# Optimization experiments

Hardware: AMD Instinct MI355X
Metric: run time of the kernel (lower is better)

The kernel has to match this reference:

```python
import jax, jax.numpy as jnp
import numpy as np

B, N, V, H = 8, 2048, 256, 1024
EPS = 1e-5
NEG = -1e9


def _layernorm(x, g, b):
    m = jnp.mean(x, axis=-1, keepdims=True)
    v = jnp.mean((x - m) ** 2, axis=-1, keepdims=True)
    return (x - m) / jnp.sqrt(v + EPS) * g + b


def setup_inputs() -> dict:
    key = jax.random.key(0)
    ks = jax.random.split(key, 10)
    tril = jnp.tril(jnp.ones((N, N), jnp.float32))
    return {
        "h": jax.random.normal(ks[0], (B, N, V), jnp.float32),
        "mask_one": tril,                      # keep causal entries
        "mask_zero": NEG * (1.0 - tril),       # -inf-ish above diagonal
        "ln_attn_g": jnp.ones((V,), jnp.float32),
        "ln_attn_b": jnp.zeros((V,), jnp.float32),
        "ln_mlp_g": jnp.ones((V,), jnp.float32),
        "ln_mlp_b": jnp.zeros((V,), jnp.float32),
        "wv": jax.random.normal(ks[1], (V,), jnp.float32),
        "wv_bos": jax.random.normal(ks[2], (V,), jnp.float32),
        "wo_w": jax.random.normal(ks[3], (V, V), jnp.float32) / np.sqrt(V),
        "qk_bos": jax.random.normal(ks[4], (V,), jnp.float32),
        "qk_previous": jax.random.normal(ks[5], (V,), jnp.float32),
        "qk_direction": jnp.ones((V,), jnp.float32),  # middel_layer=False, frozen
        "w1": jax.random.normal(ks[6], (H, V), jnp.float32) / np.sqrt(V),
        "w2": jax.random.normal(ks[7], (V, H), jnp.float32) / np.sqrt(H),
    }


def reference(h, mask_one, mask_zero, ln_attn_g, ln_attn_b, ln_mlp_g, ln_mlp_b,
              wv, wv_bos, wo_w, qk_bos, qk_previous, qk_direction, w1, w2):
    b, n, v = h.shape
    # mask blends LayerNorm only into row 0 (BOS position)
    attn_input = h.at[:, 0, :].set(_layernorm(h[:, 0, :], ln_attn_g, ln_attn_b))
    # value states: diag(wv) on positions 1.., wo(wv_bos) at position 0
    values = attn_input[:, 1:, :] * wv                      # [B, N-1, V]
    v_bos = wo_w @ wv_bos                                   # Linear(bias=False)
    values = jnp.concatenate(
        [jnp.broadcast_to(v_bos, (b, 1, v)), values], axis=1)  # [B, N, V]
    # sparse QK logits: column 0 term + sub-diagonal term, densified then masked
    col0 = (attn_input @ qk_bos) * (attn_input[:, 0, :] @ qk_direction)[:, None]  # [B, N]
    d = attn_input @ qk_previous                            # [B, N]
    qk = jnp.zeros((b, n, n), h.dtype).at[:, :, 0].add(col0)
    idx = jnp.arange(1, n)
    qk = qk.at[:, idx, idx - 1].add(d[:, 1:])               # row r, col r-1 = d[:, r]
    qk = qk * mask_one + mask_zero
    attn_out = jax.nn.softmax(qk, axis=-1) @ values         # [B, N, V]
    # FFN branch with its own BOS-only LayerNorm blend
    mlp_input = h.at[:, 0, :].set(_layernorm(h[:, 0, :], ln_mlp_g, ln_mlp_b))
    mlp_out = jax.nn.relu(mlp_input @ w1.T) @ w2.T          # [B, N, V]
    return attn_out + mlp_out
```

## Files before the change

### kernel.cpp

```cpp
#include <hip/hip_runtime.h>
#include <hip/hip_bf16.h>

#define BB 8
#define NN 2048
#define VV 256
#define HH 1024
#define CHK 64
#define RPC 32
constexpr float EPS = 1e-5f;

typedef __attribute__((ext_vector_type(4))) float floatx4;
typedef __attribute__((ext_vector_type(8))) short short8;

__device__ __forceinline__ void load_lds16(const void* g, void* l) {
    __builtin_amdgcn_global_load_lds((const __attribute__((address_space(1))) void*)g,
                                     (__attribute__((address_space(3))) void*)l, 16, 0, 0);
}
__device__ __forceinline__ float bf16s_to_f(short s) {
    unsigned u = ((unsigned)(unsigned short)s) << 16;
    return __builtin_bit_cast(float, u);
}

__global__ void prep_kernel(const float* __restrict__ h,
                            const float* __restrict__ g_attn, const float* __restrict__ b_attn,
                            const float* __restrict__ g_mlp,  const float* __restrict__ b_mlp,
                            const float* __restrict__ qk_dir,
                            const float* __restrict__ wo_w,  const float* __restrict__ wv_bos,
                            float* __restrict__ attn_row0, float* __restrict__ mlp_row0,
                            float* __restrict__ v_bos, float* __restrict__ sum0)
{
    int t = threadIdx.x;
    __shared__ float red[VV];
    if (blockIdx.x < BB) {
        int b = blockIdx.x;
        float x = h[(size_t)b * NN * VV + t];
        red[t] = x; __syncthreads();
        for (int s = 128; s > 0; s >>= 1) { if (t < s) red[t] += red[t + s]; __syncthreads(); }
        float m = red[0] * (1.0f / VV); __syncthreads();
        float xc = x - m;
        red[t] = xc * xc; __syncthreads();
        for (int s = 128; s > 0; s >>= 1) { if (t < s) red[t] += red[t + s]; __syncthreads(); }
        float var = red[0] * (1.0f / VV); __syncthreads();
        float inv = 1.0f / sqrtf(var + EPS);
        float an = xc * inv * g_attn[t] + b_attn[t];
        float mn = xc * inv * g_mlp[t] + b_mlp[t];
        attn_row0[b * VV + t] = an;
        mlp_row0[b * VV + t]  = mn;
        red[t] = an * qk_dir[t]; __syncthreads();
        for (int s = 128; s > 0; s >>= 1) { if (t < s) red[t] += red[t + s]; __syncthreads(); }
        if (t == 0) sum0[b] = red[0];
    } else {
        const float4* wp = reinterpret_cast<const float4*>(wo_w + (size_t)t * VV);
        const float4* vp = reinterpret_cast<const float4*>(wv_bos);
        float acc = 0.f;
        for (int j = 0; j < VV / 4; ++j) {
            float4 a = wp[j], b = vp[j];
            acc += a.x * b.x + a.y * b.y + a.z * b.z + a.w * b.w;
        }
        v_bos[t] = acc;
    }
}

__global__ __launch_bounds__(256) void scan_qkw_cvt_kernel(
    const float* __restrict__ h, const float* __restrict__ mlp_row0,
    const float* __restrict__ wv,
    const float* __restrict__ qk_bos, const float* __restrict__ qk_prev,
    const float* __restrict__ sum0,
    short* __restrict__ Xb,
    float* __restrict__ w0, float* __restrict__ wprev, float* __restrict__ wz,
    float* __restrict__ chunkSum)
{
    __shared__ float lds[4][VV];
    int wave = threadIdx.x >> 6, lane = threadIdx.x & 63;
    int b = blockIdx.x / CHK, c = blockIdx.x % CHK;
    int r0 = c * RPC + wave * 8;
    float4 wv4 = reinterpret_cast<const float4*>(wv)[lane];
    float4 qb4 = reinterpret_cast<const float4*>(qk_bos)[lane];
    float4 qp4 = reinterpret_cast<const float4*>(qk_prev)[lane];
    float s0b = sum0[b];
    float4 vsum = {0.f, 0.f, 0.f, 0.f};
#pragma unroll
    for (int rr = 0; rr < 8; ++rr) {
        int r = r0 + rr;
        size_t base = ((size_t)b * NN + r) * VV;
        float4 x = *reinterpret_cast<const float4*>(h + base + lane * 4);
        float4 xs = x;
        if (r == 0) xs = *reinterpret_cast<const float4*>(mlp_row0 + b * VV + lane * 4);
        __hip_bfloat16 c0 = __float2bfloat16(xs.x), c1 = __float2bfloat16(xs.y),
                       c2 = __float2bfloat16(xs.z), c3 = __float2bfloat16(xs.w);
        short4 pk;
        pk.x = *reinterpret_cast<short*>(&c0);
        pk.y = *reinterpret_cast<short*>(&c1);
        pk.z = *reinterpret_cast<short*>(&c2);
        pk.w = *reinterpret_cast<short*>(&c3);
        *reinterpret_cast<short4*>(Xb + base + lane * 4) = pk;
        if (r != 0) {
            vsum.x += bf16s_to_f(pk.x) * wv4.x; vsum.y += bf16s_to_f(pk.y) * wv4.y;
            vsum.z += bf16s_to_f(pk.z) * wv4.z; vsum.w += bf16s_to_f(pk.w) * wv4.w;
        }
        float s1 = x.x * qb4.x + x.y * qb4.y + x.z * qb4.z + x.w * qb4.w;
        float s2 = x.x * qp4.x + x.y * qp4.y + x.z * qp4.z + x.w * qp4.w;
        for (int off = 32; off > 0; off >>= 1) {
            s1 += __shfl_down(s1, off);
            s2 += __shfl_down(s2, off);
        }
        if (lane == 0) {
            int gid = b * NN + r;
            float W0, WP, WZ;
            if (r == 0) { W0 = 1.f; WP = 0.f; WZ = 0.f; }
            else if (r == 1) {
                float a = s1 * s0b + s2;
                float m = fmaxf(a, 0.f);
                float ea = expf(a - m), ez = expf(-m);
                float Z = ea + ez;
                W0 = ea / Z; WZ = ez / Z; WP = WZ;
            } else {
                float a = s1 * s0b;
                float m = fmaxf(fmaxf(a, s2), 0.f);
                float ea = expf(a - m), ed = expf(s2 - m), ez = expf(-m);
                float Z = ea + ed + (float)(r - 1) * ez;
                W0 = ea / Z; WP = ed / Z; WZ = ez / Z;
            }
            w0[gid] = W0; wprev[gid] = WP; wz[gid] = WZ;
        }
    }
    reinterpret_cast<float4*>(lds[wave])[lane] = vsum;
    __syncthreads();
    int v = threadIdx.x;
    chunkSum[((size_t)b * CHK + c) * VV + v] = lds[0][v] + lds[1][v] + lds[2][v] + lds[3][v];
}

__global__ void chunkscan_kernel(float* __restrict__ chunkSum)
{
    int b = blockIdx.x, v = threadIdx.x;
    float vals[CHK];
#pragma unroll
    for (int c = 0; c < CHK; ++c) vals[c] = chunkSum[(b * CHK + c) * VV + v];
    float run = 0.f;
#pragma unroll
    for (int c = 0; c < CHK; ++c) { float t = vals[c]; vals[c] = run; run += t; }
#pragma unroll
    for (int c = 0; c < CHK; ++c) chunkSum[(b * CHK + c) * VV + v] = vals[c];
}

__global__ __launch_bounds__(128) void attn_kernel(
    const short* __restrict__ Xb, const float* __restrict__ wv,
    const float* __restrict__ v_bos,
    const float* __restrict__ w0, const float* __restrict__ wprev,
    const float* __restrict__ wz, const float* __restrict__ chunkSum,
    float* __restrict__ out)
{
    int b = blockIdx.x / CHK, c = blockIdx.x % CHK;
    int v = threadIdx.x * 2;
    float2 wv2 = *reinterpret_cast<const float2*>(wv + v);
    float2 vb2 = *reinterpret_cast<const float2*>(v_bos + v);
    float2 S = *reinterpret_cast<const float2*>(chunkSum + (b * CHK + c) * VV + v);
    int r0 = c * RPC;
    float2 prev = {0.f, 0.f};
    if (r0 > 0) {
        short2 p = *reinterpret_cast<const short2*>(Xb + ((size_t)b * NN + r0 - 1) * VV + v);
        prev.x = bf16s_to_f(p.x) * wv2.x; prev.y = bf16s_to_f(p.y) * wv2.y;
    }
    for (int r = r0; r < r0 + RPC; ++r) {
        size_t idx = ((size_t)b * NN + r) * VV + v;
        float2 o;
        if (r == 0) {
            o = vb2;
            prev.x = 0.f; prev.y = 0.f;
        } else {
            short2 xv = *reinterpret_cast<const short2*>(Xb + idx);
            float2 val;
            val.x = bf16s_to_f(xv.x) * wv2.x; val.y = bf16s_to_f(xv.y) * wv2.y;
            S.x += val.x; S.y += val.y;
            int wi = b * NN + r;
            float W0 = w0[wi], WD = wprev[wi] - wz[wi], WZ = wz[wi];
            o.x = W0 * vb2.x + WD * prev.x + WZ * S.x;
            o.y = W0 * vb2.y + WD * prev.y + WZ * S.y;
            prev = val;
        }
        *reinterpret_cast<float2*>(out + idx) = o;
    }
}

__global__ void cvt_w_kernel(const float* __restrict__ w1, const float* __restrict__ w2,
                             __hip_bfloat16* __restrict__ w1b, __hip_bfloat16* __restrict__ w2b)
{
    int i = (blockIdx.x * blockDim.x + threadIdx.x) * 4;
    const float* src;
    __hip_bfloat16* dst;
    if (i < HH * VV) { src = w1 + i; dst = w1b + i; }
    else             { src = w2 + (i - HH * VV); dst = w2b + (i - HH * VV); }
    float4 x = *reinterpret_cast<const float4*>(src);
    dst[0] = __float2bfloat16(x.x);
    dst[1] = __float2bfloat16(x.y);
    dst[2] = __float2bfloat16(x.z);
    dst[3] = __float2bfloat16(x.w);
}

__global__ __launch_bounds__(256) void mlp_fused2(const short* __restrict__ Xb,
                                                  const short* __restrict__ w1b,
                                                  const short* __restrict__ w2b,
                                                  float* __restrict__ out)
{
    __shared__ __align__(16) short sW1[128 * 256];
    __shared__ __align__(16) short sW2[256 * 128];
    __shared__ __align__(16) short sY[64 * 128];
    int wave = threadIdx.x >> 6, lane = threadIdx.x & 63;
    int ra = lane & 15, q = lane >> 4;
    int m0 = blockIdx.x * 64;

    short8 xf[8][4];
#pragma unroll
    for (int ks = 0; ks < 8; ++ks)
#pragma unroll
        for (int i = 0; i < 4; ++i)
            xf[ks][i] = *reinterpret_cast<const short8*>(
                Xb + (size_t)(m0 + i * 16 + ra) * VV + ks * 32 + q * 8);

    floatx4 oacc[4][4];
#pragma unroll
    for (int i = 0; i < 4; ++i)
#pragma unroll
        for (int j = 0; j < 4; ++j) oacc[i][j] = floatx4{0.f, 0.f, 0.f, 0.f};

    auto stage = [&](int hc) {
#pragma unroll
        for (int it = 0; it < 16; ++it) {
            int g = wave * 16 + it;
            load_lds16(w1b + ((size_t)(hc * 128 + g * 2) * VV) + lane * 8, sW1 + g * 512);
        }
#pragma unroll
        for (int it = 0; it < 16; ++it) {
            int v4 = wave * 64 + it * 4 + (lane >> 4);
            short8 t = *reinterpret_cast<const short8*>(
                w2b + (size_t)v4 * HH + hc * 128 + (lane & 15) * 8);
            *reinterpret_cast<short8*>(sW2 + v4 * 128 + (lane & 15) * 8) = t;
        }
    };

    stage(0);
    for (int hc = 0; hc < 8; ++hc) {
        __syncthreads();
        floatx4 yacc[4][2];
#pragma unroll
        for (int i = 0; i < 4; ++i) { yacc[i][0] = floatx4{0,0,0,0}; yacc[i][1] = floatx4{0,0,0,0}; }
#pragma unroll
        for (int ks = 0; ks < 8; ++ks) {
#pragma unroll
            for (int j = 0; j < 2; ++j) {
                int n = wave * 32 + j * 16 + ra;
                short8 bfr = *reinterpret_cast<const short8*>(sW1 + n * 256 + ks * 32 + q * 8);
#pragma unroll
                for (int i = 0; i < 4; ++i)
                    yacc[i][j] = __builtin_amdgcn_mfma_f32_16x16x32_bf16(xf[ks][i], bfr, yacc[i][j], 0, 0, 0);
            }
        }
#pragma unroll
        for (int i = 0; i < 4; ++i)
#pragma unroll
            for (int j = 0; j < 2; ++j)
#pragma unroll
                for (int reg = 0; reg < 4; ++reg) {
                    int row = i * 16 + q * 4 + reg;
                    int col = wave * 32 + j * 16 + ra;
                    __hip_bfloat16 hb = __float2bfloat16(fmaxf(yacc[i][j][reg], 0.f));
                    sY[row * 128 + col] = *reinterpret_cast<short*>(&hb);
                }
        __syncthreads();

#pragma unroll
        for (int kk = 0; kk < 4; ++kk) {
            short8 a2[4];
#pragma unroll
            for (int i = 0; i < 4; ++i)
                a2[i] = *reinterpret_cast<const short8*>(sY + (i * 16 + ra) * 128 + kk * 32 + q * 8);
#pragma unroll
            for (int j = 0; j < 4; ++j) {
                int n = wave * 64 + j * 16 + ra;
                short8 b2 = *reinterpret_cast<const short8*>(sW2 + n * 128 + kk * 32 + q * 8);
#pragma unroll
                for (int i = 0; i < 4; ++i)
                    oacc[i][j] = __builtin_amdgcn_mfma_f32_16x16x32_bf16(a2[i], b2, oacc[i][j], 0, 0, 0);
            }
        }
        __syncthreads();
        if (hc < 7) stage(hc + 1);
    }

#pragma unroll
    for (int i = 0; i < 4; ++i)
#pragma unroll
        for (int j = 0; j < 4; ++j)
#pragma unroll
            for (int reg = 0; reg < 4; ++reg) {
                int row = m0 + i * 16 + q * 4 + reg;
                int col = wave * 64 + j * 16 + ra;
                out[(size_t)row * VV + col] += oacc[i][j][reg];
            }
}

extern "C" void kernel_launch(void* const* d_in, const int* in_sizes, int n_in,
                              void* d_out, int out_size, void* d_ws, size_t ws_size,
                              hipStream_t stream)
{
    const float* h        = (const float*)d_in[0];
    const float* ln_attn_g = (const float*)d_in[3];
    const float* ln_attn_b = (const float*)d_in[4];
    const float* ln_mlp_g  = (const float*)d_in[5];
    const float* ln_mlp_b  = (const float*)d_in[6];
    const float* wv        = (const float*)d_in[7];
    const float* wv_bos    = (const float*)d_in[8];
    const float* wo_w      = (const float*)d_in[9];
    const float* qk_bos    = (const float*)d_in[10];
    const float* qk_prev   = (const float*)d_in[11];
    const float* qk_dir    = (const float*)d_in[12];
    const float* w1        = (const float*)d_in[13];
    const float* w2        = (const float*)d_in[14];
    float* out = (float*)d_out;

    float* attn_row0 = (float*)d_ws;
    float* mlp_row0  = attn_row0 + BB * VV;
    float* v_bos     = mlp_row0 + BB * VV;
    float* sum0      = v_bos + VV;
    float* w0        = sum0 + 8;
    float* wprev     = w0 + BB * NN;
    float* wzz       = wprev + BB * NN;
    float* chunkSum  = wzz + BB * NN;
    short* Xb            = (short*)(chunkSum + BB * CHK * VV);
    __hip_bfloat16* w1b  = (__hip_bfloat16*)(Xb + (size_t)BB * NN * VV);
    __hip_bfloat16* w2b  = w1b + HH * VV;

    prep_kernel<<<BB + 1, 256, 0, stream>>>(h, ln_attn_g, ln_attn_b, ln_mlp_g, ln_mlp_b,
                                            qk_dir, wo_w, wv_bos,
                                            attn_row0, mlp_row0, v_bos, sum0);
    cvt_w_kernel<<<(2 * HH * VV / 4) / 256, 256, 0, stream>>>(w1, w2, w1b, w2b);
    scan_qkw_cvt_kernel<<<BB * CHK, 256, 0, stream>>>(h, mlp_row0, wv, qk_bos, qk_prev,
                                                      sum0, Xb, w0, wprev, wzz, chunkSum);
    chunkscan_kernel<<<BB, 256, 0, stream>>>(chunkSum);
    attn_kernel<<<BB * CHK, 128, 0, stream>>>(Xb, wv, v_bos, w0, wprev, wzz, chunkSum, out);
    mlp_fused2<<<256, 256, 0, stream>>>(Xb, (const short*)w1b, (const short*)w2b, out);
}
```

Baseline: 190.8 us.

## Double-buffer MLP weight staging with XOR-swizzled LDS and 8 waves

```diff
diff --git a/kernel.cpp b/kernel.cpp
--- a/kernel.cpp
+++ b/kernel.cpp
@@ -197,104 +197,111 @@
     dst[3] = __float2bfloat16(x.w);
 }
 
-__global__ __launch_bounds__(256) void mlp_fused2(const short* __restrict__ Xb,
+__global__ __launch_bounds__(512) void mlp_fused3(const short* __restrict__ Xb,
                                                   const short* __restrict__ w1b,
                                                   const short* __restrict__ w2b,
                                                   float* __restrict__ out)
 {
-    __shared__ __align__(16) short sW1[128 * 256];
-    __shared__ __align__(16) short sW2[256 * 128];
-    __shared__ __align__(16) short sY[64 * 128];
+    __shared__ __align__(16) short sW1[2][64 * 256];
+    __shared__ __align__(16) short sW2[2][256 * 64];
+    __shared__ __align__(16) short sY[64 * 64];
     int wave = threadIdx.x >> 6, lane = threadIdx.x & 63;
+    int wm = wave >> 2, wn = wave & 3;
     int ra = lane & 15, q = lane >> 4;
     int m0 = blockIdx.x * 64;
 
-    short8 xf[8][4];
+    short8 xf[8][2];
 #pragma unroll
     for (int ks = 0; ks < 8; ++ks)
 #pragma unroll
-        for (int i = 0; i < 4; ++i)
+        for (int i = 0; i < 2; ++i)
             xf[ks][i] = *reinterpret_cast<const short8*>(
-                Xb + (size_t)(m0 + i * 16 + ra) * VV + ks * 32 + q * 8);
-
-    floatx4 oacc[4][4];
-#pragma unroll
-    for (int i = 0; i < 4; ++i)
+                Xb + (size_t)(m0 + wm * 32 + i * 16 + ra) * VV + ks * 32 + q * 8);
+
+    floatx4 oacc[2][4];
+#pragma unroll
+    for (int i = 0; i < 2; ++i)
 #pragma unroll
         for (int j = 0; j < 4; ++j) oacc[i][j] = floatx4{0.f, 0.f, 0.f, 0.f};
 
-    auto stage = [&](int hc) {
-#pragma unroll
-        for (int it = 0; it < 16; ++it) {
-            int g = wave * 16 + it;
-            load_lds16(w1b + ((size_t)(hc * 128 + g * 2) * VV) + lane * 8, sW1 + g * 512);
-        }
-#pragma unroll
-        for (int it = 0; it < 16; ++it) {
-            int v4 = wave * 64 + it * 4 + (lane >> 4);
-            short8 t = *reinterpret_cast<const short8*>(
-                w2b + (size_t)v4 * HH + hc * 128 + (lane & 15) * 8);
-            *reinterpret_cast<short8*>(sW2 + v4 * 128 + (lane & 15) * 8) = t;
+    auto stage = [&](int hc, int buf) {
+#pragma unroll
+        for (int it = 0; it < 4; ++it) {
+            int g = wave * 4 + it;
+            int n = g * 2 + (lane >> 5);
+            int slot = lane & 31;
+            load_lds16(w1b + (size_t)(hc * 64 + n) * VV + (slot ^ (n & 7)) * 8,
+                       &sW1[buf][g * 512]);
+        }
+#pragma unroll
+        for (int it = 0; it < 4; ++it) {
+            int g = wave * 4 + it;
+            int v = g * 8 + (lane >> 3);
+            int slot = lane & 7;
+            load_lds16(w2b + (size_t)v * HH + hc * 64 + (slot ^ (v & 7)) * 8,
+                       &sW2[buf][g * 512]);
         }
     };
 
-    stage(0);
-    for (int hc = 0; hc < 8; ++hc) {
+    stage(0, 0);
+    for (int hc = 0; hc < 16; ++hc) {
+        int p = hc & 1;
         __syncthreads();
-        floatx4 yacc[4][2];
-#pragma unroll
-        for (int i = 0; i < 4; ++i) { yacc[i][0] = floatx4{0,0,0,0}; yacc[i][1] = floatx4{0,0,0,0}; }
+        if (hc < 15) stage(hc + 1, p ^ 1);
+
+        floatx4 yacc[2];
+        yacc[0] = floatx4{0.f, 0.f, 0.f, 0.f};
+        yacc[1] = floatx4{0.f, 0.f, 0.f, 0.f};
+        int nb = wn * 16 + ra;
 #pragma unroll
         for (int ks = 0; ks < 8; ++ks) {
-#pragma unroll
-            for (int j = 0; j < 2; ++j) {
-                int n = wave * 32 + j * 16 + ra;
-                short8 bfr = *reinterpret_cast<const short8*>(sW1 + n * 256 + ks * 32 + q * 8);
-#pragma unroll
-                for (int i = 0; i < 4; ++i)
-                    yacc[i][j] = __builtin_amdgcn_mfma_f32_16x16x32_bf16(xf[ks][i], bfr, yacc[i][j], 0, 0, 0);
-            }
-        }
-#pragma unroll
-        for (int i = 0; i < 4; ++i)
-#pragma unroll
-            for (int j = 0; j < 2; ++j)
-#pragma unroll
-                for (int reg = 0; reg < 4; ++reg) {
-                    int row = i * 16 + q * 4 + reg;
-                    int col = wave * 32 + j * 16 + ra;
-                    __hip_bfloat16 hb = __float2bfloat16(fmaxf(yacc[i][j][reg], 0.f));
-                    sY[row * 128 + col] = *reinterpret_cast<short*>(&hb);
-                }
+            short8 bfr = *reinterpret_cast<const short8*>(
+                &sW1[p][nb * 256 + (((ks * 4 + q) ^ (ra & 7)) * 8)]);
+#pragma unroll
+            for (int i = 0; i < 2; ++i)
+                yacc[i] = __builtin_amdgcn_mfma_f32_16x16x32_bf16(xf[ks][i], bfr, yacc[i], 0, 0, 0);
+        }
+#pragma unroll
+        for (int i = 0; i < 2; ++i)
+#pragma unroll
+            for (int reg = 0; reg < 4; ++reg) {
+                int m = wm * 32 + i * 16 + q * 4 + reg;
+                int ke = wn * 16 + ra;
+                __hip_bfloat16 hb = __float2bfloat16(fmaxf(yacc[i][reg], 0.f));
+                sY[m * 64 + (((ke >> 3) ^ (m & 7)) * 8) + (ke & 7)] =
+                    *reinterpret_cast<short*>(&hb);
+            }
         __syncthreads();
 
 #pragma unroll
-        for (int kk = 0; kk < 4; ++kk) {
-            short8 a2[4];
-#pragma unroll
-            for (int i = 0; i < 4; ++i)
-                a2[i] = *reinterpret_cast<const short8*>(sY + (i * 16 + ra) * 128 + kk * 32 + q * 8);
+        for (int kk = 0; kk < 2; ++kk) {
+            short8 a2[2];
+#pragma unroll
+            for (int i = 0; i < 2; ++i) {
+                int m = wm * 32 + i * 16 + ra;
+                a2[i] = *reinterpret_cast<const short8*>(
+                    &sY[m * 64 + (((kk * 4 + q) ^ (ra & 7)) * 8)]);
+            }
 #pragma unroll
             for (int j = 0; j < 4; ++j) {
-                int n = wave * 64 + j * 16 + ra;
-                short8 b2 = *reinterpret_cast<const short8*>(sW2 + n * 128 + kk * 32 + q * 8);
-#pragma unroll
-                for (int i = 0; i < 4; ++i)
+                int v = wn * 64 + j * 16 + ra;
+                short8 b2 = *reinterpret_cast<const short8*>(
+                    &sW2[p][v * 64 + (((kk * 4 + q) ^ (ra & 7)) * 8)]);
+#pragma unroll
+                for (int i = 0; i < 2; ++i)
                     oacc[i][j] = __builtin_amdgcn_mfma_f32_16x16x32_bf16(a2[i], b2, oacc[i][j], 0, 0, 0);
             }
         }
-        __syncthreads();
-        if (hc < 7) stage(hc + 1);
-    }
-
-#pragma unroll
-    for (int i = 0; i < 4; ++i)
+    }
+
+#pragma unroll
+    for (int i = 0; i < 2; ++i)
 #pragma unroll
         for (int j = 0; j < 4; ++j)
 #pragma unroll
             for (int reg = 0; reg < 4; ++reg) {
-                int row = m0 + i * 16 + q * 4 + reg;
-                int col = wave * 64 + j * 16 + ra;
+                int row = m0 + wm * 32 + i * 16 + q * 4 + reg;
+                int col = wn * 64 + j * 16 + ra;
                 out[(size_t)row * VV + col] += oacc[i][j][reg];
             }
 }
@@ -338,5 +345,5 @@
                                                       sum0, Xb, w0, wprev, wzz, chunkSum);
     chunkscan_kernel<<<BB, 256, 0, stream>>>(chunkSum);
     attn_kernel<<<BB * CHK, 128, 0, stream>>>(Xb, wv, v_bos, w0, wprev, wzz, chunkSum, out);
-    mlp_fused2<<<256, 256, 0, stream>>>(Xb, (const short*)w1b, (const short*)w2b, out);
-}
+    mlp_fused3<<<256, 512, 0, stream>>>(Xb, (const short*)w1b, (const short*)w2b, out);
+}
```

Result: faster. 172.3 us (-9.7%).
